# Kernel optimization log

Measured on AMD Instinct MI355X. Metric: run time of the kernel, lower is better.

## Reference

```python
import jax, jax.numpy as jnp
import numpy as np


def cmul(a, b):
    # complex multiply on (..., 2) real/imag pairs
    ar, ai = a[..., 0], a[..., 1]
    br, bi = b[..., 0], b[..., 1]
    return jnp.stack([ar * br - ai * bi, ar * bi + ai * br], axis=-1)


def butterfly_apply(x, diag, subdiag, superdiag, k):
    # x: [B, n, 2]; tridiagonal-at-offset-k complex matrix applied to x.
    # diag: [n, 2]; subdiag/superdiag padded to [n, 2], first n-k entries used.
    n = x.shape[-2]
    out = cmul(diag, x)
    out = out.at[..., k:, :].add(cmul(subdiag[: n - k], x[..., : n - k, :]))
    out = out.at[..., : n - k, :].add(cmul(superdiag[: n - k], x[..., k:, :]))
    return out


def block_perm(x, logit, s):
    # Soft block permutation: within each contiguous block of size s,
    # mix identity with even-odd separation (prob p0), then mix each half
    # with its reversal (probs p1, p2). Acts identically on real & imag.
    B, n, _ = x.shape
    p = jax.nn.sigmoid(logit)
    y = x.reshape(B, n // s, s, 2)
    eo = jnp.concatenate([y[:, :, 0::2, :], y[:, :, 1::2, :]], axis=2)
    y = (1 - p[0]) * y + p[0] * eo
    h = s // 2
    first = (1 - p[1]) * y[:, :, :h, :] + p[1] * jnp.flip(y[:, :, :h, :], axis=2)
    second = (1 - p[2]) * y[:, :, h:, :] + p[2] * jnp.flip(y[:, :, h:, :], axis=2)
    return jnp.concatenate([first, second], axis=2).reshape(B, n, 2)


def trifat_forward(x, perm_logits, diags, subdiags, superdiags, bias):
    B, n = x.shape
    depth, m = diags.shape[0], diags.shape[1]
    perm_sizes = [n >> i for i in range(m - 1)][::-1]  # 4, 8, ..., n
    # real_to_complex: zero imaginary part
    xc = jnp.stack([x, jnp.zeros_like(x)], axis=-1)  # [B, n, 2]
    for d in range(depth):
        for j, s in enumerate(perm_sizes):
            xc = block_perm(xc, perm_logits[d, j], s)
        for i in range(m):
            k = n >> (i + 1)  # offsets n/2, n/4, ..., 1
            xc = butterfly_apply(xc, diags[d, i], subdiags[d, i], superdiags[d, i], k)
    return xc[..., 0] + bias  # take real part, add bias


def setup_inputs() -> dict:
    key = jax.random.key(0)
    ks = jax.random.split(key, 6)
    B, n, depth = 4096, 1024, 2
    m = int(np.log2(n))
    return {
        "x": jax.random.normal(ks[0], (B, n), jnp.float32),
        "perm_logits": jax.random.normal(ks[1], (depth, m - 1, 3), jnp.float32),
        "diags": jax.random.normal(ks[2], (depth, m, n, 2), jnp.float32),
        "subdiags": jax.random.normal(ks[3], (depth, m, n, 2), jnp.float32),
        "superdiags": jax.random.normal(ks[4], (depth, m, n, 2), jnp.float32),
        "bias": jnp.zeros((n,), jnp.float32),
    }


def reference(x, perm_logits, diags, subdiags, superdiags, bias):
    return trifat_forward(x, perm_logits, diags, subdiags, superdiags, bias)
```

## Files before the change

kernel.cpp:

```cpp
#include <hip/hip_runtime.h>

#define N 1024
#define THREADS 256
#define EPT 4

__device__ __forceinline__ float2* run_pipeline(
    float2* bufA, float2* bufB, int tid,
    const float* __restrict__ logits,
    const float* __restrict__ diags,
    const float* __restrict__ subd,
    const float* __restrict__ supd)
{
    float2* src = bufA;
    float2* dst = bufB;

    for (int d = 0; d < 2; ++d) {
        for (int j = 0; j < 9; ++j) {
            const int s = 4 << j;
            const int h = s >> 1;
            const float* lg = logits + (d * 9 + j) * 3;
            const float p0 = 1.0f / (1.0f + expf(-lg[0]));
            const float p1 = 1.0f / (1.0f + expf(-lg[1]));
            const float p2 = 1.0f / (1.0f + expf(-lg[2]));
#pragma unroll
            for (int e = 0; e < EPT; ++e) {
                const int idx = tid + e * THREADS;
                const int base = idx & ~(s - 1);
                const int t = idx & (s - 1);
                const bool lo = (t < h);

                const int eo_t = lo ? (2 * t) : (2 * (t - h) + 1);
                const float2 xt  = src[idx];
                const float2 xeo = src[base + eo_t];
                float2 yt;
                yt.x = xt.x + p0 * (xeo.x - xt.x);
                yt.y = xt.y + p0 * (xeo.y - xt.y);

                const int tm = lo ? (h - 1 - t) : (s + h - 1 - t);
                const float psel = lo ? p1 : p2;
                const int eo_m = (tm < h) ? (2 * tm) : (2 * (tm - h) + 1);
                const float2 xm   = src[base + tm];
                const float2 xmeo = src[base + eo_m];
                float2 ym;
                ym.x = xm.x + p0 * (xmeo.x - xm.x);
                ym.y = xm.y + p0 * (xmeo.y - xm.y);

                float2 o;
                o.x = yt.x + psel * (ym.x - yt.x);
                o.y = yt.y + psel * (ym.y - yt.y);
                dst[idx] = o;
            }
            __syncthreads();
            float2* tmp = src; src = dst; dst = tmp;
        }
        for (int i = 0; i < 10; ++i) {
            const int k = N >> (i + 1);
            const float2* Dg = (const float2*)(diags + (size_t)((d * 10 + i) * N) * 2);
            const float2* Sb = (const float2*)(subd  + (size_t)((d * 10 + i) * N) * 2);
            const float2* Sp = (const float2*)(supd  + (size_t)((d * 10 + i) * N) * 2);
#pragma unroll
            for (int e = 0; e < EPT; ++e) {
                const int idx = tid + e * THREADS;
                const float2 xv = src[idx];
                const float2 dg = Dg[idx];
                float2 o;
                o.x = dg.x * xv.x - dg.y * xv.y;
                o.y = dg.x * xv.y + dg.y * xv.x;
                if (idx >= k) {
                    const float2 xs = src[idx - k];
                    const float2 sb = Sb[idx - k];
                    o.x += sb.x * xs.x - sb.y * xs.y;
                    o.y += sb.x * xs.y + sb.y * xs.x;
                }
                if (idx < N - k) {
                    const float2 xp = src[idx + k];
                    const float2 sp = Sp[idx];
                    o.x += sp.x * xp.x - sp.y * xp.y;
                    o.y += sp.x * xp.y + sp.y * xp.x;
                }
                dst[idx] = o;
            }
            __syncthreads();
            float2* tmp = src; src = dst; dst = tmp;
        }
    }
    return src;
}

__global__ __launch_bounds__(THREADS) void trifat_kernel(
    const float* __restrict__ x,
    const float* __restrict__ logits,
    const float* __restrict__ diags,
    const float* __restrict__ subd,
    const float* __restrict__ supd,
    const float* __restrict__ bias,
    float* __restrict__ out,
    int B)
{
    __shared__ float2 bufA[N];
    __shared__ float2 bufB[N];

    const int row = blockIdx.x;
    const int tid = threadIdx.x;
    if (row >= B) return;

    const float* xr = x + (size_t)row * N;
#pragma unroll
    for (int e = 0; e < EPT; ++e) {
        int idx = tid + e * THREADS;
        bufA[idx] = make_float2(xr[idx], 0.0f);
    }
    __syncthreads();

    float2* res = run_pipeline(bufA, bufB, tid, logits, diags, subd, supd);

    float* orow = out + (size_t)row * N;
#pragma unroll
    for (int e = 0; e < EPT; ++e) {
        int idx = tid + e * THREADS;
        orow[idx] = res[idx].x + bias[idx];
    }
}

__device__ __forceinline__ unsigned short f2bf_rne(float f) {
    unsigned int u = __float_as_uint(f);
    unsigned int r = u + 0x7fffu + ((u >> 16) & 1u);
    return (unsigned short)(r >> 16);
}

#define TBW 512
#define NB_BUILD 512

__global__ __launch_bounds__(TBW) void prep_kernel(
    const float* __restrict__ logits,
    const float* __restrict__ diags,
    const float* __restrict__ subd,
    const float* __restrict__ supd,
    const float* __restrict__ x,
    unsigned short* __restrict__ Bt,
    unsigned short* __restrict__ A2)
{
    __shared__ __align__(16) float2 buf[2][2][N];

    const int tid = threadIdx.x;

    if (blockIdx.x >= NB_BUILD) {
        const int cb = blockIdx.x - NB_BUILD;
        const size_t base4 = (size_t)cb * 4096;
#pragma unroll
        for (int r = 0; r < 8; ++r) {
            const size_t g4 = base4 + r * 512 + tid;
            const float4 v = *(const float4*)(x + g4 * 4);
            ushort4 o;
            o.x = f2bf_rne(v.x);
            o.y = f2bf_rne(v.y);
            o.z = f2bf_rne(v.z);
            o.w = f2bf_rne(v.w);
            *(ushort4*)(A2 + g4 * 4) = o;
        }
        return;
    }

    const int j0 = blockIdx.x * 2;
    const int t = tid;

#pragma unroll
    for (int b = 0; b < 2; ++b)
#pragma unroll
        for (int v = 0; v < 2; ++v)
#pragma unroll
            for (int e = 0; e < 2; ++e)
                buf[b][v][tid + e * TBW] = make_float2(0.0f, 0.0f);
    __syncthreads();
    if (tid < 2) buf[0][tid][j0 + tid] = make_float2(1.0f, 0.0f);
    __syncthreads();

    int sb = 0;
    for (int d = 0; d < 2; ++d) {
        for (int jp = 0; jp < 9; ++jp) {
            const int s = 4 << jp;
            const int h = s >> 1;
            const int hh = s >> 2;
            const float* lg = logits + (d * 9 + jp) * 3;
            const float p0 = 1.0f / (1.0f + expf(-lg[0]));
            const float p1 = 1.0f / (1.0f + expf(-lg[1]));
            const float p2 = 1.0f / (1.0f + expf(-lg[2]));

            int w = -1, base = 0;
            if (d == 0) {
                if (tid < (s >> 1)) {
                    w = tid;
                    base = (j0 >> (jp + 2)) << (jp + 2);
                }
            } else {
                w = tid & ((s >> 1) - 1);
                base = (tid >> (jp + 1)) << (jp + 2);
            }

            if (w >= 0) {
                int tt, tm;
                float psel;
                if (w < hh) { tt = w;         tm = h - 1 - w;  psel = p1; }
                else        { const int u = w - hh; tt = h + u; tm = s - 1 - u; psel = p2; }

                const int eot = (tt < h) ? (2 * tt) : (2 * (tt - h) + 1);
                const int eom = (tm < h) ? (2 * tm) : (2 * (tm - h) + 1);

#pragma unroll
                for (int v = 0; v < 2; ++v) {
                    const float2* src = buf[sb][v];
                    float2* dst = buf[sb ^ 1][v];

                    const float2 xt = src[base + tt], xet = src[base + eot];
                    const float2 xm = src[base + tm], xem = src[base + eom];
                    float2 yt, ym;
                    yt.x = xt.x + p0 * (xet.x - xt.x);
                    yt.y = xt.y + p0 * (xet.y - xt.y);
                    ym.x = xm.x + p0 * (xem.x - xm.x);
                    ym.y = xm.y + p0 * (xem.y - xm.y);

                    float2 ot, om;
                    ot.x = yt.x + psel * (ym.x - yt.x);
                    ot.y = yt.y + psel * (ym.y - yt.y);
                    om.x = ym.x + psel * (yt.x - ym.x);
                    om.y = ym.y + psel * (yt.y - ym.y);
                    dst[base + tt] = ot;
                    dst[base + tm] = om;
                }
            }
            __syncthreads();
            sb ^= 1;
        }

        float4 dg4, sb4, sp4;
        {
            const float4* Dg4 = (const float4*)(diags + (size_t)((d * 10) * N) * 2);
            const float4* Sb4 = (const float4*)(subd  + (size_t)((d * 10) * N) * 2);
            const float4* Sp4 = (const float4*)(supd  + (size_t)((d * 10) * N) * 2);
            dg4 = Dg4[t];
            sb4 = (t >= 256) ? Sb4[t - 256] : make_float4(0.f, 0.f, 0.f, 0.f);
            sp4 = (t < 256)  ? Sp4[t]       : make_float4(0.f, 0.f, 0.f, 0.f);
        }
        for (int i = 0; i < 9; ++i) {
            const int k = N >> (i + 1);
            const int k2 = k >> 1;

            float4 dg4n, sb4n, sp4n;
            if (i < 8) {
                const int kn2 = k2 >> 1;
                const float4* Dg4 = (const float4*)(diags + (size_t)((d * 10 + i + 1) * N) * 2);
                const float4* Sb4 = (const float4*)(subd  + (size_t)((d * 10 + i + 1) * N) * 2);
                const float4* Sp4 = (const float4*)(supd  + (size_t)((d * 10 + i + 1) * N) * 2);
                dg4n = Dg4[t];
                sb4n = (t >= kn2)       ? Sb4[t - kn2] : make_float4(0.f, 0.f, 0.f, 0.f);
                sp4n = (t < 512 - kn2)  ? Sp4[t]       : make_float4(0.f, 0.f, 0.f, 0.f);
            }

            const bool has_sb = (t >= k2);
            const bool has_sp = (t < 512 - k2);
#pragma unroll
            for (int v = 0; v < 2; ++v) {
                const float2* src = buf[sb][v];
                const float4 xv = *(const float4*)(&src[2 * t]);
                float4 o;
                o.x = dg4.x * xv.x - dg4.y * xv.y;
                o.y = dg4.x * xv.y + dg4.y * xv.x;
                o.z = dg4.z * xv.z - dg4.w * xv.w;
                o.w = dg4.z * xv.w + dg4.w * xv.z;
                if (has_sb) {
                    const float4 xs = *(const float4*)(&src[2 * t - k]);
                    o.x += sb4.x * xs.x - sb4.y * xs.y;
                    o.y += sb4.x * xs.y + sb4.y * xs.x;
                    o.z += sb4.z * xs.z - sb4.w * xs.w;
                    o.w += sb4.z * xs.w + sb4.w * xs.z;
                }
                if (has_sp) {
                    const float4 xp = *(const float4*)(&src[2 * t + k]);
                    o.x += sp4.x * xp.x - sp4.y * xp.y;
                    o.y += sp4.x * xp.y + sp4.y * xp.x;
                    o.z += sp4.z * xp.z - sp4.w * xp.w;
                    o.w += sp4.z * xp.w + sp4.w * xp.z;
                }
                *(float4*)(&buf[sb ^ 1][v][2 * t]) = o;
            }
            __syncthreads();
            sb ^= 1;
            if (i < 8) { dg4 = dg4n; sb4 = sb4n; sp4 = sp4n; }
        }
        {
            const float2* Dg = (const float2*)(diags + (size_t)((d * 10 + 9) * N) * 2);
            const float2* Sb = (const float2*)(subd  + (size_t)((d * 10 + 9) * N) * 2);
            const float2* Sp = (const float2*)(supd  + (size_t)((d * 10 + 9) * N) * 2);
            const int i0 = 2 * t, i1 = 2 * t + 1;
            const float2 dg0 = Dg[i0], dg1 = Dg[i1];
            const float2 sb0 = (t >= 1) ? Sb[i0 - 1] : make_float2(0.f, 0.f);
            const float2 sb1 = Sb[i0];
            const float2 sp0 = Sp[i0];
            const float2 sp1 = (t < 511) ? Sp[i1] : make_float2(0.f, 0.f);
#pragma unroll
            for (int v = 0; v < 2; ++v) {
                const float2* src = buf[sb][v];
                const float2 x0 = src[i0], x1 = src[i1];
                float2 o0, o1;
                o0.x = dg0.x * x0.x - dg0.y * x0.y;
                o0.y = dg0.x * x0.y + dg0.y * x0.x;
                o1.x = dg1.x * x1.x - dg1.y * x1.y;
                o1.y = dg1.x * x1.y + dg1.y * x1.x;
                if (t >= 1) {
                    const float2 xs = src[i0 - 1];
                    o0.x += sb0.x * xs.x - sb0.y * xs.y;
                    o0.y += sb0.x * xs.y + sb0.y * xs.x;
                }
                o1.x += sb1.x * x0.x - sb1.y * x0.y;
                o1.y += sb1.x * x0.y + sb1.y * x0.x;
                o0.x += sp0.x * x1.x - sp0.y * x1.y;
                o0.y += sp0.x * x1.y + sp0.y * x1.x;
                if (t < 511) {
                    const float2 xp = src[i1 + 1];
                    o1.x += sp1.x * xp.x - sp1.y * xp.y;
                    o1.y += sp1.x * xp.y + sp1.y * xp.x;
                }
                float4 ow;
                ow.x = o0.x; ow.y = o0.y; ow.z = o1.x; ow.w = o1.y;
                *(float4*)(&buf[sb ^ 1][v][i0]) = ow;
            }
            __syncthreads();
            sb ^= 1;
        }
    }

#pragma unroll
    for (int v = 0; v < 2; ++v)
#pragma unroll
        for (int e = 0; e < 2; ++e) {
            const int idx = tid + e * TBW;
            Bt[(size_t)idx * N + (j0 + v)] = f2bf_rne(buf[sb][v][idx].x);
        }
}

typedef __attribute__((ext_vector_type(8))) __bf16 bf16x8;
typedef __attribute__((ext_vector_type(4))) float f32x4;

#define GLB(p) ((const __attribute__((address_space(1))) void*)(p))
#define LDS(p) ((__attribute__((address_space(3))) void*)(p))

__global__ __launch_bounds__(THREADS) void gemm_bf16(
    const unsigned short* __restrict__ A2,
    const unsigned short* __restrict__ Bt,
    const float* __restrict__ bias,
    float* __restrict__ out)
{
    __shared__ __align__(16) unsigned short As[64 * 64];
    __shared__ __align__(16) unsigned short Bs[64 * 64];

    const int m0 = blockIdx.x * 64;
    const int n0 = blockIdx.y * 64;
    const int tid = threadIdx.x;
    const int wave = tid >> 6, lane = tid & 63;
    const int wm = (wave >> 1) * 32, wn = (wave & 1) * 32;
    const int lrow = lane & 15, q = lane >> 4;
    const int r7 = lrow & 7;

    f32x4 acc[2][2] = {};

    for (int kt = 0; kt < 16; ++kt) {
        const int k0 = kt * 64;
        __syncthreads();
        {
            const unsigned short* gA = A2 + (size_t)m0 * N + k0;
            const unsigned short* gB = Bt + (size_t)n0 * N + k0;
#pragma unroll
            for (int r = 0; r < 2; ++r) {
                const int s = r * 256 + tid;
                const int row = s >> 3;
                const int gl = (s & 7) ^ (row & 7);
                __builtin_amdgcn_global_load_lds(GLB(gA + (size_t)row * N + gl * 8),
                                                 LDS(As + s * 8), 16, 0, 0);
                __builtin_amdgcn_global_load_lds(GLB(gB + (size_t)row * N + gl * 8),
                                                 LDS(Bs + s * 8), 16, 0, 0);
            }
        }
        __syncthreads();

#pragma unroll
        for (int kk = 0; kk < 64; kk += 32) {
            const int pg = ((kk >> 3) + q) ^ r7;
            bf16x8 a[2], b[2];
#pragma unroll
            for (int mi = 0; mi < 2; ++mi)
                a[mi] = *(const bf16x8*)(As + (wm + mi * 16 + lrow) * 64 + pg * 8);
#pragma unroll
            for (int ni = 0; ni < 2; ++ni)
                b[ni] = *(const bf16x8*)(Bs + (wn + ni * 16 + lrow) * 64 + pg * 8);
#pragma unroll
            for (int mi = 0; mi < 2; ++mi)
#pragma unroll
                for (int ni = 0; ni < 2; ++ni)
                    acc[mi][ni] = __builtin_amdgcn_mfma_f32_16x16x32_bf16(
                        a[mi], b[ni], acc[mi][ni], 0, 0, 0);
        }
    }

#pragma unroll
    for (int ni = 0; ni < 2; ++ni) {
        const int col = n0 + wn + ni * 16 + lrow;
        const float bv = bias[col];
#pragma unroll
        for (int mi = 0; mi < 2; ++mi)
#pragma unroll
            for (int r = 0; r < 4; ++r) {
                const int row = m0 + wm + mi * 16 + q * 4 + r;
                out[(size_t)row * N + col] = acc[mi][ni][r] + bv;
            }
    }
}

extern "C" void kernel_launch(void* const* d_in, const int* in_sizes, int n_in,
                              void* d_out, int out_size, void* d_ws, size_t ws_size,
                              hipStream_t stream) {
    const float* x      = (const float*)d_in[0];
    const float* logits = (const float*)d_in[1];
    const float* diags  = (const float*)d_in[2];
    const float* subd   = (const float*)d_in[3];
    const float* supd   = (const float*)d_in[4];
    const float* bias   = (const float*)d_in[5];
    float* out = (float*)d_out;

    const int B = in_sizes[0] / N;

    const size_t off_Bt = 0;
    const size_t off_A2 = 2u * 1024 * 1024;
    const size_t need   = off_A2 + (size_t)B * N * 2;

    if (ws_size >= need && B == 4096) {
        unsigned short* Bt = (unsigned short*)((char*)d_ws + off_Bt);
        unsigned short* A2 = (unsigned short*)((char*)d_ws + off_A2);

        prep_kernel<<<dim3(NB_BUILD + 256), dim3(TBW), 0, stream>>>(
            logits, diags, subd, supd, x, Bt, A2);
        gemm_bf16<<<dim3(B / 64, 16), dim3(THREADS), 0, stream>>>(A2, Bt, bias, out);
    } else {
        trifat_kernel<<<dim3(B), dim3(THREADS), 0, stream>>>(
            x, logits, diags, subd, supd, bias, out, B);
    }
}
```

Before: 126.5 us.

## Build one basis column per 256-thread block in prep kernel

The matrix-building part of the prep kernel now has each 256-thread block build a single basis column instead of two columns per 512-thread block, which halves shared memory per block and doubles the block count. Sigmoids of the logits are computed once into shared memory instead of per stage, and the diagonal-load prefetching is dropped in favor of direct loads inside each stage. The aim is higher occupancy and more blocks to hide the per-stage barrier latency. In exchange, each coefficient load is issued twice as many times in total and the x-conversion blocks each do more work.

After: 125.9 us. Within noise of the previous version (-0.4%).

```diff
diff --git a/kernel.cpp b/kernel.cpp
--- a/kernel.cpp
+++ b/kernel.cpp
@@ -128,10 +128,10 @@
     return (unsigned short)(r >> 16);
 }
 
-#define TBW 512
-#define NB_BUILD 512
-
-__global__ __launch_bounds__(TBW) void prep_kernel(
+#define TB 256
+#define NBUILD 1024
+
+__global__ __launch_bounds__(TB, 5) void prep_kernel(
     const float* __restrict__ logits,
     const float* __restrict__ diags,
     const float* __restrict__ subd,
@@ -140,16 +140,17 @@
     unsigned short* __restrict__ Bt,
     unsigned short* __restrict__ A2)
 {
-    __shared__ __align__(16) float2 buf[2][2][N];
+    __shared__ __align__(16) float2 buf[2][N];
+    __shared__ float sig[54];
 
     const int tid = threadIdx.x;
 
-    if (blockIdx.x >= NB_BUILD) {
-        const int cb = blockIdx.x - NB_BUILD;
+    if (blockIdx.x >= NBUILD) {
+        const int cb = blockIdx.x - NBUILD;
         const size_t base4 = (size_t)cb * 4096;
 #pragma unroll
-        for (int r = 0; r < 8; ++r) {
-            const size_t g4 = base4 + r * 512 + tid;
+        for (int r = 0; r < 16; ++r) {
+            const size_t g4 = base4 + (size_t)r * TB + tid;
             const float4 v = *(const float4*)(x + g4 * 4);
             ushort4 o;
             o.x = f2bf_rne(v.x);
@@ -161,55 +162,52 @@
         return;
     }
 
-    const int j0 = blockIdx.x * 2;
-    const int t = tid;
+    const int j = blockIdx.x;
 
 #pragma unroll
     for (int b = 0; b < 2; ++b)
 #pragma unroll
-        for (int v = 0; v < 2; ++v)
-#pragma unroll
-            for (int e = 0; e < 2; ++e)
-                buf[b][v][tid + e * TBW] = make_float2(0.0f, 0.0f);
+        for (int e = 0; e < 4; ++e)
+            buf[b][tid + e * TB] = make_float2(0.0f, 0.0f);
+    if (tid < 54) sig[tid] = 1.0f / (1.0f + __expf(-logits[tid]));
     __syncthreads();
-    if (tid < 2) buf[0][tid][j0 + tid] = make_float2(1.0f, 0.0f);
+    if (tid == 0) buf[0][j] = make_float2(1.0f, 0.0f);
     __syncthreads();
 
-    int sb = 0;
+    int pb = 0;
     for (int d = 0; d < 2; ++d) {
         for (int jp = 0; jp < 9; ++jp) {
             const int s = 4 << jp;
             const int h = s >> 1;
             const int hh = s >> 2;
-            const float* lg = logits + (d * 9 + jp) * 3;
-            const float p0 = 1.0f / (1.0f + expf(-lg[0]));
-            const float p1 = 1.0f / (1.0f + expf(-lg[1]));
-            const float p2 = 1.0f / (1.0f + expf(-lg[2]));
-
-            int w = -1, base = 0;
-            if (d == 0) {
-                if (tid < (s >> 1)) {
-                    w = tid;
-                    base = (j0 >> (jp + 2)) << (jp + 2);
-                }
-            } else {
-                w = tid & ((s >> 1) - 1);
-                base = (tid >> (jp + 1)) << (jp + 2);
-            }
-
-            if (w >= 0) {
-                int tt, tm;
-                float psel;
-                if (w < hh) { tt = w;         tm = h - 1 - w;  psel = p1; }
-                else        { const int u = w - hh; tt = h + u; tm = s - 1 - u; psel = p2; }
-
-                const int eot = (tt < h) ? (2 * tt) : (2 * (tt - h) + 1);
-                const int eom = (tm < h) ? (2 * tm) : (2 * (tm - h) + 1);
-
-#pragma unroll
-                for (int v = 0; v < 2; ++v) {
-                    const float2* src = buf[sb][v];
-                    float2* dst = buf[sb ^ 1][v];
+            const float p0 = sig[(d * 9 + jp) * 3 + 0];
+            const float p1 = sig[(d * 9 + jp) * 3 + 1];
+            const float p2 = sig[(d * 9 + jp) * 3 + 2];
+            const float2* src = buf[pb];
+            float2* dst = buf[pb ^ 1];
+
+#pragma unroll
+            for (int e = 0; e < 2; ++e) {
+                const int task = tid + e * TB;
+                int w = -1, base = 0;
+                if (d == 0) {
+                    if (task < h) {
+                        w = task;
+                        base = (j >> (jp + 2)) << (jp + 2);
+                    }
+                } else {
+                    w = task & (h - 1);
+                    base = (task >> (jp + 1)) << (jp + 2);
+                }
+
+                if (w >= 0) {
+                    int tt, tm;
+                    float psel;
+                    if (w < hh) { tt = w;              tm = h - 1 - w;  psel = p1; }
+                    else        { const int u = w - hh; tt = h + u; tm = s - 1 - u; psel = p2; }
+
+                    const int eot = (tt < h) ? (2 * tt) : (2 * (tt - h) + 1);
+                    const int eom = (tm < h) ? (2 * tm) : (2 * (tm - h) + 1);
 
                     const float2 xt = src[base + tt], xet = src[base + eot];
                     const float2 xm = src[base + tm], xem = src[base + eom];
@@ -229,84 +227,76 @@
                 }
             }
             __syncthreads();
-            sb ^= 1;
-        }
-
-        float4 dg4, sb4, sp4;
-        {
-            const float4* Dg4 = (const float4*)(diags + (size_t)((d * 10) * N) * 2);
-            const float4* Sb4 = (const float4*)(subd  + (size_t)((d * 10) * N) * 2);
-            const float4* Sp4 = (const float4*)(supd  + (size_t)((d * 10) * N) * 2);
-            dg4 = Dg4[t];
-            sb4 = (t >= 256) ? Sb4[t - 256] : make_float4(0.f, 0.f, 0.f, 0.f);
-            sp4 = (t < 256)  ? Sp4[t]       : make_float4(0.f, 0.f, 0.f, 0.f);
-        }
+            pb ^= 1;
+        }
+
         for (int i = 0; i < 9; ++i) {
             const int k = N >> (i + 1);
             const int k2 = k >> 1;
-
-            float4 dg4n, sb4n, sp4n;
-            if (i < 8) {
-                const int kn2 = k2 >> 1;
-                const float4* Dg4 = (const float4*)(diags + (size_t)((d * 10 + i + 1) * N) * 2);
-                const float4* Sb4 = (const float4*)(subd  + (size_t)((d * 10 + i + 1) * N) * 2);
-                const float4* Sp4 = (const float4*)(supd  + (size_t)((d * 10 + i + 1) * N) * 2);
-                dg4n = Dg4[t];
-                sb4n = (t >= kn2)       ? Sb4[t - kn2] : make_float4(0.f, 0.f, 0.f, 0.f);
-                sp4n = (t < 512 - kn2)  ? Sp4[t]       : make_float4(0.f, 0.f, 0.f, 0.f);
-            }
-
-            const bool has_sb = (t >= k2);
-            const bool has_sp = (t < 512 - k2);
-#pragma unroll
-            for (int v = 0; v < 2; ++v) {
-                const float2* src = buf[sb][v];
-                const float4 xv = *(const float4*)(&src[2 * t]);
+            const float4* Dg4 = (const float4*)(diags + (size_t)((d * 10 + i) * N) * 2);
+            const float4* Sb4 = (const float4*)(subd  + (size_t)((d * 10 + i) * N) * 2);
+            const float4* Sp4 = (const float4*)(supd  + (size_t)((d * 10 + i) * N) * 2);
+            const float2* src = buf[pb];
+            float2* dst = buf[pb ^ 1];
+
+#pragma unroll
+            for (int e = 0; e < 2; ++e) {
+                const int g = tid + e * TB;
+                const bool hsb = (g >= k2);
+                const bool hsp = (g < 512 - k2);
+                const float4 dg4 = Dg4[g];
+                const float4 sb4 = hsb ? Sb4[g - k2] : make_float4(0.f, 0.f, 0.f, 0.f);
+                const float4 sp4 = hsp ? Sp4[g]      : make_float4(0.f, 0.f, 0.f, 0.f);
+
+                const float4 xv = *(const float4*)(&src[2 * g]);
                 float4 o;
                 o.x = dg4.x * xv.x - dg4.y * xv.y;
                 o.y = dg4.x * xv.y + dg4.y * xv.x;
                 o.z = dg4.z * xv.z - dg4.w * xv.w;
                 o.w = dg4.z * xv.w + dg4.w * xv.z;
-                if (has_sb) {
-                    const float4 xs = *(const float4*)(&src[2 * t - k]);
+                if (hsb) {
+                    const float4 xs = *(const float4*)(&src[2 * g - k]);
                     o.x += sb4.x * xs.x - sb4.y * xs.y;
                     o.y += sb4.x * xs.y + sb4.y * xs.x;
                     o.z += sb4.z * xs.z - sb4.w * xs.w;
                     o.w += sb4.z * xs.w + sb4.w * xs.z;
                 }
-                if (has_sp) {
-                    const float4 xp = *(const float4*)(&src[2 * t + k]);
+                if (hsp) {
+                    const float4 xp = *(const float4*)(&src[2 * g + k]);
                     o.x += sp4.x * xp.x - sp4.y * xp.y;
                     o.y += sp4.x * xp.y + sp4.y * xp.x;
                     o.z += sp4.z * xp.z - sp4.w * xp.w;
                     o.w += sp4.z * xp.w + sp4.w * xp.z;
                 }
-                *(float4*)(&buf[sb ^ 1][v][2 * t]) = o;
+                *(float4*)(&dst[2 * g]) = o;
             }
             __syncthreads();
-            sb ^= 1;
-            if (i < 8) { dg4 = dg4n; sb4 = sb4n; sp4 = sp4n; }
+            pb ^= 1;
         }
         {
             const float2* Dg = (const float2*)(diags + (size_t)((d * 10 + 9) * N) * 2);
             const float2* Sb = (const float2*)(subd  + (size_t)((d * 10 + 9) * N) * 2);
             const float2* Sp = (const float2*)(supd  + (size_t)((d * 10 + 9) * N) * 2);
-            const int i0 = 2 * t, i1 = 2 * t + 1;
-            const float2 dg0 = Dg[i0], dg1 = Dg[i1];
-            const float2 sb0 = (t >= 1) ? Sb[i0 - 1] : make_float2(0.f, 0.f);
-            const float2 sb1 = Sb[i0];
-            const float2 sp0 = Sp[i0];
-            const float2 sp1 = (t < 511) ? Sp[i1] : make_float2(0.f, 0.f);
-#pragma unroll
-            for (int v = 0; v < 2; ++v) {
-                const float2* src = buf[sb][v];
+            const float2* src = buf[pb];
+            float2* dst = buf[pb ^ 1];
+
+#pragma unroll
+            for (int e = 0; e < 2; ++e) {
+                const int g = tid + e * TB;
+                const int i0 = 2 * g, i1 = 2 * g + 1;
+                const float2 dg0 = Dg[i0], dg1 = Dg[i1];
+                const float2 sb0 = (g >= 1)  ? Sb[i0 - 1] : make_float2(0.f, 0.f);
+                const float2 sb1 = Sb[i0];
+                const float2 sp0 = Sp[i0];
+                const float2 sp1 = (g < 511) ? Sp[i1]     : make_float2(0.f, 0.f);
+
                 const float2 x0 = src[i0], x1 = src[i1];
                 float2 o0, o1;
                 o0.x = dg0.x * x0.x - dg0.y * x0.y;
                 o0.y = dg0.x * x0.y + dg0.y * x0.x;
                 o1.x = dg1.x * x1.x - dg1.y * x1.y;
                 o1.y = dg1.x * x1.y + dg1.y * x1.x;
-                if (t >= 1) {
+                if (g >= 1) {
                     const float2 xs = src[i0 - 1];
                     o0.x += sb0.x * xs.x - sb0.y * xs.y;
                     o0.y += sb0.x * xs.y + sb0.y * xs.x;
@@ -315,27 +305,25 @@
                 o1.y += sb1.x * x0.y + sb1.y * x0.x;
                 o0.x += sp0.x * x1.x - sp0.y * x1.y;
                 o0.y += sp0.x * x1.y + sp0.y * x1.x;
-                if (t < 511) {
+                if (g < 511) {
                     const float2 xp = src[i1 + 1];
                     o1.x += sp1.x * xp.x - sp1.y * xp.y;
                     o1.y += sp1.x * xp.y + sp1.y * xp.x;
                 }
                 float4 ow;
                 ow.x = o0.x; ow.y = o0.y; ow.z = o1.x; ow.w = o1.y;
-                *(float4*)(&buf[sb ^ 1][v][i0]) = ow;
+                *(float4*)(&dst[i0]) = ow;
             }
             __syncthreads();
-            sb ^= 1;
-        }
-    }
-
-#pragma unroll
-    for (int v = 0; v < 2; ++v)
-#pragma unroll
-        for (int e = 0; e < 2; ++e) {
-            const int idx = tid + e * TBW;
-            Bt[(size_t)idx * N + (j0 + v)] = f2bf_rne(buf[sb][v][idx].x);
-        }
+            pb ^= 1;
+        }
+    }
+
+#pragma unroll
+    for (int e = 0; e < 4; ++e) {
+        const int idx = tid + e * TB;
+        Bt[(size_t)idx * N + j] = f2bf_rne(buf[pb][idx].x);
+    }
 }
 
 typedef __attribute__((ext_vector_type(8))) __bf16 bf16x8;
@@ -436,7 +424,7 @@
         unsigned short* Bt = (unsigned short*)((char*)d_ws + off_Bt);
         unsigned short* A2 = (unsigned short*)((char*)d_ws + off_A2);
 
-        prep_kernel<<<dim3(NB_BUILD + 256), dim3(TBW), 0, stream>>>(
+        prep_kernel<<<dim3(NBUILD + 256), dim3(TB), 0, stream>>>(
             logits, diags, subd, supd, x, Bt, A2);
         gemm_bf16<<<dim3(B / 64, 16), dim3(THREADS), 0, stream>>>(A2, Bt, bias, out);
     } else {
```
